# Optimization experiments

Hardware: AMD Instinct MI355X
Metric: run time of the kernel (lower is better)

## Reference

```python
import jax, jax.numpy as jnp
import numpy as np

B, C, H, W = 64, 256, 48, 48
NH = 8          # num_heads
DH = C // NH    # per-head dim = 32
DFF = 2 * C     # FFN hidden = 512 (hard-coded d_ffn=feature_dim*2)
M = 64          # base_class_num
EPS_NORM = 1e-5
EPS_LN = 1e-5


def setup_inputs() -> dict:
    key = jax.random.key(0)
    ks = jax.random.split(key, 12)
    s = 0.02
    return {
        "feature": jax.random.normal(ks[0], (B, C, H, W), jnp.float32),
        "base_class_weight": jax.random.normal(ks[1], (M, C), jnp.float32),
        # 1x1-conv projections (weight [out,in], bias [out])
        "wq": jax.random.normal(ks[2], (C, C), jnp.float32) * s,
        "bq": jnp.zeros((C,), jnp.float32),
        "wk": jax.random.normal(ks[3], (C, C), jnp.float32) * s,
        "bk": jnp.zeros((C,), jnp.float32),
        "wv": jax.random.normal(ks[4], (C, C), jnp.float32) * s,
        "bv": jnp.zeros((C,), jnp.float32),
        "wm": jax.random.normal(ks[5], (C, C), jnp.float32) * s,
        "bm": jnp.zeros((C,), jnp.float32),
        # FFN_MLP
        "w1": jax.random.normal(ks[6], (DFF, C), jnp.float32) * s,
        "b1": jnp.zeros((DFF,), jnp.float32),
        "w2": jax.random.normal(ks[7], (C, DFF), jnp.float32) * s,
        "b2": jnp.zeros((C,), jnp.float32),
        "gamma": jnp.ones((C,), jnp.float32),
        "beta": jnp.zeros((C,), jnp.float32),
    }


def reference(feature, base_class_weight, wq, bq, wk, bk, wv, bv, wm, bm,
              w1, b1, w2, b2, gamma, beta):
    b, c, h, w = feature.shape
    n = h * w
    feat_cn = feature.reshape(b, c, n)                 # [B,c,N]  (q input, channel-first)
    feat_nc = feat_cn.transpose(0, 2, 1)               # [B,N,c]  ('feature' var in torch)
    kv_cm = jnp.broadcast_to(base_class_weight.T[None], (b, c, M))  # [B,c,M]

    # 1x1-conv projections then split channels as [dim, heads] (dim outer, per torch view)
    qp = (jnp.einsum('oc,bcn->bon', wq, feat_cn) + bq[None, :, None]).reshape(b, DH, NH, n)
    kp = (jnp.einsum('oc,bcm->bom', wk, kv_cm) + bk[None, :, None]).reshape(b, DH, NH, M)
    vp = (jnp.einsum('oc,bcm->bom', wv, kv_cm) + bv[None, :, None]).reshape(b, DH, NH, M)

    scores = jnp.einsum('bdhn,bdhm->bhnm', qp, kp) / jnp.sqrt(jnp.float32(DH))
    prob = jax.nn.softmax(scores, axis=-1)             # [B,H,N,M]
    x = jnp.einsum('bhnm,bdhm->bdhn', prob, vp)        # [B,dim,H,N]
    merged = jnp.einsum('oc,bcn->bon', wm, x.reshape(b, c, n)) + bm[None, :, None]  # [B,c,N]

    # SFTA cosine re-weighting
    aligned = merged.transpose(0, 2, 1)                # [B,N,c]
    an = aligned / (jnp.linalg.norm(aligned, axis=-1, keepdims=True) + EPS_NORM)
    fn = feat_nc / (jnp.linalg.norm(feat_nc, axis=-1, keepdims=True) + EPS_NORM)
    cos = jnp.sum(an * fn, axis=-1)                    # [B,N]
    out = feat_nc * (cos + 1.0)[:, :, None]            # [B,N,c]

    # FFN_MLP (dropout = identity in eval) + residual + LayerNorm
    h1 = jax.nn.relu(jnp.einsum('bnc,fc->bnf', out, w1) + b1)
    src2 = jnp.einsum('bnf,cf->bnc', h1, w2) + b2
    src = out + src2
    mu = jnp.mean(src, axis=-1, keepdims=True)
    var = jnp.mean(jnp.square(src - mu), axis=-1, keepdims=True)
    src = (src - mu) / jnp.sqrt(var + EPS_LN) * gamma + beta

    return src.transpose(0, 2, 1).reshape(b, c, h, w)
```

## Files before the change

### kernel.cpp

```cpp
#include <hip/hip_runtime.h>

#define Bc   64
#define Cc   256
#define Nn   2304
#define DFFf 512
#define Mm   64
#define NTILE 64
#define NTB   36

typedef __bf16 bf16_t;
typedef __bf16 bf16x8 __attribute__((ext_vector_type(8)));
typedef __bf16 bf16x4 __attribute__((ext_vector_type(4)));
typedef float  f32x4  __attribute__((ext_vector_type(4)));
typedef float  f32x2  __attribute__((ext_vector_type(2)));

__device__ __forceinline__ bf16_t cvt(float f) { return (bf16_t)f; }

__device__ __forceinline__ f32x4 mfma16(bf16x8 a, bf16x8 b, f32x4 c) {
    return __builtin_amdgcn_mfma_f32_16x16x32_bf16(a, b, c, 0, 0, 0);
}

__global__ void kv_kernel(const float* __restrict__ wk, const float* __restrict__ bk,
                          const float* __restrict__ wv, const float* __restrict__ bv,
                          const float* __restrict__ bcw,
                          float* __restrict__ Kout, float* __restrict__ Vout) {
    int c = blockIdx.x;
    int m = threadIdx.x;
    const float* wkr = wk + c * Cc;
    const float* wvr = wv + c * Cc;
    const float* br  = bcw + m * Cc;
    float aK = 0.f, aV = 0.f;
    #pragma unroll 8
    for (int i = 0; i < Cc; ++i) {
        float bcv = br[i];
        aK = fmaf(wkr[i], bcv, aK);
        aV = fmaf(wvr[i], bcv, aV);
    }
    Kout[c * Mm + m] = aK + bk[c];
    Vout[c * Mm + m] = aV + bv[c];
}

__global__ void pack_kernel(const float* __restrict__ wq, const float* __restrict__ bq,
                            const float* __restrict__ wm, const float* __restrict__ w1,
                            const float* __restrict__ w2,
                            const float* __restrict__ Kf32, const float* __restrict__ Vf32,
                            bf16_t* __restrict__ wqf, bf16_t* __restrict__ wmf,
                            bf16_t* __restrict__ w1f, bf16_t* __restrict__ w2f,
                            bf16_t* __restrict__ Kf, bf16_t* __restrict__ Vf,
                            float* __restrict__ bqp) {
    int idx = blockIdx.x * 256 + threadIdx.x;
    if (idx < 65536) {
        int e = idx;
        int j = e & 7, lane = (e >> 3) & 63, rs = e >> 9;
        int ks = rs & 7, rt = rs >> 3;
        int rho = lane & 15;
        int h = rt >> 1, rtl = rt & 1;
        int d = 8 * (rho >> 2) + 4 * rtl + (rho & 3);
        int k  = ks * 32 + (lane >> 4) * 8 + j;
        int c  = d * 8 + h;
        wqf[e] = cvt(wq[c * 256 + k]);
    } else if (idx < 131072) {
        int e = idx - 65536;
        int j = e & 7, lane = (e >> 3) & 63, rs = e >> 9;
        int ks = rs & 7, rt = rs >> 3;
        int o = rt * 16 + (lane & 15);
        int k = ks * 32 + (lane >> 4) * 8 + j;
        int c = (k & 31) * 8 + (k >> 5);
        wmf[e] = cvt(wm[o * 256 + c]);
    } else if (idx < 262144) {
        int e = idx - 131072;
        int j = e & 7, lane = (e >> 3) & 63, rs = e >> 9;
        int ks = rs & 7, rt = rs >> 3;
        w1f[e] = cvt(w1[(rt * 16 + (lane & 15)) * 256 + ks * 32 + (lane >> 4) * 8 + j]);
    } else if (idx < 393216) {
        int e = idx - 262144;
        int j = e & 7, lane = (e >> 3) & 63, rs = e >> 9;
        int ks = rs & 15, rt = rs >> 4;
        w2f[e] = cvt(w2[(rt * 16 + (lane & 15)) * 512 + ks * 32 + (lane >> 4) * 8 + j]);
    } else if (idx < 409600) {
        int e = idx - 393216;
        int j = e & 7, lane = (e >> 3) & 63, hm = e >> 9;
        int mt = hm & 3, h = hm >> 2;
        int lid = lane & 15;
        int d = (lane >> 4) * 8 + j;
        int m = 32 * (mt >> 1) + 4 * (mt & 1) + 8 * (lid >> 2) + (lid & 3);
        Kf[e] = cvt(Kf32[(d * 8 + h) * 64 + m]);
    } else if (idx < 425984) {
        int e = idx - 409600;
        int j = e & 7, lane = (e >> 3) & 63, x = e >> 9;
        int ks = x & 1, rt = (x >> 1) & 1, h = x >> 2;
        int d = rt * 16 + (lane & 15), m = ks * 32 + (lane >> 4) * 8 + j;
        Vf[e] = cvt(Vf32[(d * 8 + h) * 64 + m]);
    } else if (idx < 426240) {
        int op = idx - 425984;
        int c = (op & 31) * 8 + (op >> 5);
        bqp[op] = bq[c];
    }
}

__global__ __launch_bounds__(1024, 8) void sfta_mfma(
    const float* __restrict__ feat,
    const bf16_t* __restrict__ wqf, const float* __restrict__ bqp,
    const bf16_t* __restrict__ wmf, const float* __restrict__ bm,
    const bf16_t* __restrict__ w1f, const float* __restrict__ b1,
    const bf16_t* __restrict__ w2f, const float* __restrict__ b2,
    const bf16_t* __restrict__ Kf,  const bf16_t* __restrict__ Vf,
    const float* __restrict__ gam,  const float* __restrict__ bet,
    float* __restrict__ out) {
    __shared__ __align__(16) bf16_t sFeat[64 * 264];
    __shared__ __align__(16) bf16_t sQX[64 * 264];
    __shared__ float sRed[3][64][18];

    const int t    = threadIdx.x;
    const int wid  = t >> 6;
    const int lane = t & 63;
    const int quad = lane >> 4;
    const int lid  = lane & 15;
    const int h    = wid >> 1;
    const int rtl  = wid & 1;
    const int b    = blockIdx.y;
    const int n0   = blockIdx.x * NTILE;
    const size_t baseF = (size_t)b * Cc * Nn + n0;

    {
        int cb = t >> 4;
        int nb = (t & 15) * 4;
        #pragma unroll
        for (int i = 0; i < 4; ++i) {
            int c = i * 64 + cb;
            const float4 f4 = *(const float4*)(feat + baseF + (size_t)c * Nn + nb);
            sFeat[(nb + 0) * 264 + c] = cvt(f4.x);
            sFeat[(nb + 1) * 264 + c] = cvt(f4.y);
            sFeat[(nb + 2) * 264 + c] = cvt(f4.z);
            sFeat[(nb + 3) * 264 + c] = cvt(f4.w);
        }
    }
    __syncthreads();

    {
        f32x4 qacc[4];
        #pragma unroll
        for (int nt = 0; nt < 4; ++nt) qacc[nt] = (f32x4){0.f, 0.f, 0.f, 0.f};
        #pragma unroll
        for (int ks = 0; ks < 8; ++ks) {
            bf16x8 a = *(const bf16x8*)(wqf + ((wid * 8 + ks) * 64 + lane) * 8);
            #pragma unroll
            for (int nt = 0; nt < 4; ++nt) {
                bf16x8 bfr = *(const bf16x8*)(sFeat + (nt * 16 + lid) * 264 + ks * 32 + quad * 8);
                qacc[nt] = mfma16(a, bfr, qacc[nt]);
            }
        }
        const float4 qb = *(const float4*)(bqp + h * 32 + quad * 8 + rtl * 4);
        #pragma unroll
        for (int nt = 0; nt < 4; ++nt) {
            bf16x4 o;
            o[0] = cvt(qacc[nt][0] + qb.x);
            o[1] = cvt(qacc[nt][1] + qb.y);
            o[2] = cvt(qacc[nt][2] + qb.z);
            o[3] = cvt(qacc[nt][3] + qb.w);
            *(bf16x4*)(sQX + (nt * 16 + lid) * 264 + h * 32 + quad * 8 + rtl * 4) = o;
        }
    }
    __syncthreads();

    {
        bf16x8 kb[4];
        #pragma unroll
        for (int mt = 0; mt < 4; ++mt)
            kb[mt] = *(const bf16x8*)(Kf + ((h * 4 + mt) * 64 + lane) * 8);
        const float scl2 = 0.17677669529663687f * 1.4426950408889634f;
        #pragma unroll 1
        for (int u = 0; u < 2; ++u) {
            int g = rtl * 2 + u;
            float p[16];
            {
                bf16x8 aq = *(const bf16x8*)(sQX + (g * 16 + lid) * 264 + h * 32 + quad * 8);
                #pragma unroll
                for (int mt = 0; mt < 4; ++mt) {
                    f32x4 z = {0.f, 0.f, 0.f, 0.f};
                    f32x4 sc = mfma16(kb[mt], aq, z);
                    #pragma unroll
                    for (int r = 0; r < 4; ++r) p[mt * 4 + r] = sc[r] * scl2;
                }
            }
            float mx = p[0];
            #pragma unroll
            for (int i = 1; i < 16; ++i) mx = fmaxf(mx, p[i]);
            mx = fmaxf(mx, __shfl_xor(mx, 16));
            mx = fmaxf(mx, __shfl_xor(mx, 32));
            float s = 0.f;
            #pragma unroll
            for (int i = 0; i < 16; ++i) { p[i] = exp2f(p[i] - mx); s += p[i]; }
            s += __shfl_xor(s, 16);
            s += __shfl_xor(s, 32);
            float inv = 1.f / s;
            bf16x8 bp[2];
            #pragma unroll
            for (int ks = 0; ks < 2; ++ks)
                #pragma unroll
                for (int jj = 0; jj < 8; ++jj)
                    bp[ks][jj] = cvt(p[(2 * ks + (jj >> 2)) * 4 + (jj & 3)] * inv);
            #pragma unroll
            for (int rv = 0; rv < 2; ++rv) {
                f32x4 x = {0.f, 0.f, 0.f, 0.f};
                bf16x8 va0 = *(const bf16x8*)(Vf + ((h * 4 + rv * 2 + 0) * 64 + lane) * 8);
                x = mfma16(va0, bp[0], x);
                bf16x8 va1 = *(const bf16x8*)(Vf + ((h * 4 + rv * 2 + 1) * 64 + lane) * 8);
                x = mfma16(va1, bp[1], x);
                bf16x4 o;
                #pragma unroll
                for (int r = 0; r < 4; ++r) o[r] = cvt(x[r]);
                *(bf16x4*)(sQX + (g * 16 + lid) * 264 + h * 32 + rv * 16 + quad * 4) = o;
            }
        }
    }
    __syncthreads();

    float pmf[4], pmm[4], pff[4];
    {
        f32x4 acc[4];
        #pragma unroll
        for (int nt = 0; nt < 4; ++nt) acc[nt] = (f32x4){0.f, 0.f, 0.f, 0.f};
        #pragma unroll
        for (int ks = 0; ks < 8; ++ks) {
            bf16x8 a = *(const bf16x8*)(wmf + ((wid * 8 + ks) * 64 + lane) * 8);
            #pragma unroll
            for (int nt = 0; nt < 4; ++nt) {
                bf16x8 bx = *(const bf16x8*)(sQX + (nt * 16 + lid) * 264 + ks * 32 + quad * 8);
                acc[nt] = mfma16(a, bx, acc[nt]);
            }
        }
        const float4 bmv = *(const float4*)(bm + wid * 16 + quad * 4);
        #pragma unroll
        for (int nt = 0; nt < 4; ++nt) { pmf[nt] = 0.f; pmm[nt] = 0.f; pff[nt] = 0.f; }
        #pragma unroll
        for (int nt = 0; nt < 4; ++nt) {
            bf16x4 f4 = *(const bf16x4*)(sFeat + (nt * 16 + lid) * 264 + wid * 16 + quad * 4);
            #pragma unroll
            for (int r = 0; r < 4; ++r) {
                float m = acc[nt][r] + ((const float*)&bmv)[r];
                float f = (float)f4[r];
                pmf[nt] = fmaf(m, f, pmf[nt]);
                pmm[nt] = fmaf(m, m, pmm[nt]);
                pff[nt] = fmaf(f, f, pff[nt]);
            }
        }
    }
    #pragma unroll
    for (int nt = 0; nt < 4; ++nt) {
        pmf[nt] += __shfl_xor(pmf[nt], 16); pmf[nt] += __shfl_xor(pmf[nt], 32);
        pmm[nt] += __shfl_xor(pmm[nt], 16); pmm[nt] += __shfl_xor(pmm[nt], 32);
        pff[nt] += __shfl_xor(pff[nt], 16); pff[nt] += __shfl_xor(pff[nt], 32);
    }
    if (lane < 16) {
        #pragma unroll
        for (int nt = 0; nt < 4; ++nt) {
            sRed[0][nt * 16 + lane][wid] = pmf[nt];
            sRed[1][nt * 16 + lane][wid] = pmm[nt];
            sRed[2][nt * 16 + lane][wid] = pff[nt];
        }
    }
    __syncthreads();

    {
        int row = wid * 4 + quad;
        float smf = 0.f, smm = 0.f, sff = 0.f;
        #pragma unroll
        for (int k2 = 0; k2 < 8; ++k2) {
            f32x2 a0 = *(const f32x2*)(&sRed[0][row][k2 * 2]);
            f32x2 a1 = *(const f32x2*)(&sRed[1][row][k2 * 2]);
            f32x2 a2 = *(const f32x2*)(&sRed[2][row][k2 * 2]);
            smf += a0[0] + a0[1];
            smm += a1[0] + a1[1];
            sff += a2[0] + a2[1];
        }
        float scale = smf / ((sqrtf(smm) + 1e-5f) * (sqrtf(sff) + 1e-5f)) + 1.f;
        bf16_t* frow = sFeat + row * 264 + lid * 16;
        #pragma unroll
        for (int i = 0; i < 2; ++i) {
            bf16x8* pp = (bf16x8*)(frow + i * 8);
            bf16x8 v = *pp;
            #pragma unroll
            for (int e = 0; e < 8; ++e) v[e] = cvt((float)v[e] * scale);
            *pp = v;
        }
    }
    __syncthreads();

    f32x4 acc2[4];
    #pragma unroll
    for (int nt = 0; nt < 4; ++nt) acc2[nt] = (f32x4){0.f, 0.f, 0.f, 0.f};
    #pragma unroll 1
    for (int c = 0; c < 2; ++c) {
        int rt1 = c * 16 + wid;
        {
            f32x4 a1[4];
            #pragma unroll
            for (int nt = 0; nt < 4; ++nt) a1[nt] = (f32x4){0.f, 0.f, 0.f, 0.f};
            #pragma unroll
            for (int ks = 0; ks < 8; ++ks) {
                bf16x8 a = *(const bf16x8*)(w1f + ((rt1 * 8 + ks) * 64 + lane) * 8);
                #pragma unroll
                for (int nt = 0; nt < 4; ++nt) {
                    bf16x8 bfr = *(const bf16x8*)(sFeat + (nt * 16 + lid) * 264 + ks * 32 + quad * 8);
                    a1[nt] = mfma16(a, bfr, a1[nt]);
                }
            }
            const float4 b1v = *(const float4*)(b1 + rt1 * 16 + quad * 4);
            #pragma unroll
            for (int nt = 0; nt < 4; ++nt) {
                bf16x4 o;
                o[0] = cvt(fmaxf(a1[nt][0] + b1v.x, 0.f));
                o[1] = cvt(fmaxf(a1[nt][1] + b1v.y, 0.f));
                o[2] = cvt(fmaxf(a1[nt][2] + b1v.z, 0.f));
                o[3] = cvt(fmaxf(a1[nt][3] + b1v.w, 0.f));
                *(bf16x4*)(sQX + (nt * 16 + lid) * 264 + wid * 16 + quad * 4) = o;
            }
        }
        __syncthreads();
        #pragma unroll
        for (int kk = 0; kk < 8; ++kk) {
            bf16x8 a = *(const bf16x8*)(w2f + ((wid * 16 + c * 8 + kk) * 64 + lane) * 8);
            #pragma unroll
            for (int nt = 0; nt < 4; ++nt) {
                bf16x8 bh = *(const bf16x8*)(sQX + (nt * 16 + lid) * 264 + kk * 32 + quad * 8);
                acc2[nt] = mfma16(a, bh, acc2[nt]);
            }
        }
        __syncthreads();
    }

    float ps[4] = {0.f, 0.f, 0.f, 0.f}, pq[4] = {0.f, 0.f, 0.f, 0.f};
    {
        const float4 b2v = *(const float4*)(b2 + wid * 16 + quad * 4);
        #pragma unroll
        for (int nt = 0; nt < 4; ++nt) {
            bf16x4 f4 = *(const bf16x4*)(sFeat + (nt * 16 + lid) * 264 + wid * 16 + quad * 4);
            #pragma unroll
            for (int r = 0; r < 4; ++r) {
                float v = acc2[nt][r] + ((const float*)&b2v)[r] + (float)f4[r];
                acc2[nt][r] = v;
                ps[nt] += v;
                pq[nt] = fmaf(v, v, pq[nt]);
            }
        }
    }
    #pragma unroll
    for (int nt = 0; nt < 4; ++nt) {
        ps[nt] += __shfl_xor(ps[nt], 16); ps[nt] += __shfl_xor(ps[nt], 32);
        pq[nt] += __shfl_xor(pq[nt], 16); pq[nt] += __shfl_xor(pq[nt], 32);
    }
    if (lane < 16) {
        #pragma unroll
        for (int nt = 0; nt < 4; ++nt) {
            sRed[0][nt * 16 + lane][wid] = ps[nt];
            sRed[1][nt * 16 + lane][wid] = pq[nt];
        }
    }
    __syncthreads();

    float* op = out + baseF;
    const float4 gv = *(const float4*)(gam + wid * 16 + quad * 4);
    const float4 bv = *(const float4*)(bet + wid * 16 + quad * 4);
    #pragma unroll
    for (int nt = 0; nt < 4; ++nt) {
        int row = nt * 16 + lid;
        float s = 0.f, q = 0.f;
        #pragma unroll
        for (int k2 = 0; k2 < 2; ++k2) {
            f32x2 a0 = *(const f32x2*)(&sRed[0][row][quad * 4 + k2 * 2]);
            f32x2 a1 = *(const f32x2*)(&sRed[1][row][quad * 4 + k2 * 2]);
            s += a0[0] + a0[1];
            q += a1[0] + a1[1];
        }
        s += __shfl_xor(s, 16); s += __shfl_xor(s, 32);
        q += __shfl_xor(q, 16); q += __shfl_xor(q, 32);
        float mu   = s * (1.f / 256.f);
        float rstd = rsqrtf(q * (1.f / 256.f) - mu * mu + 1e-5f);
        int ob = wid * 16 + quad * 4;
        #pragma unroll
        for (int r = 0; r < 4; ++r) {
            float y = (acc2[nt][r] - mu) * rstd * ((const float*)&gv)[r]
                      + ((const float*)&bv)[r];
            op[(size_t)(ob + r) * Nn + row] = y;
        }
    }
}

extern "C" void kernel_launch(void* const* d_in, const int* in_sizes, int n_in,
                              void* d_out, int out_size, void* d_ws, size_t ws_size,
                              hipStream_t stream) {
    const float* feature = (const float*)d_in[0];
    const float* bcw     = (const float*)d_in[1];
    const float* wq = (const float*)d_in[2];  const float* bq = (const float*)d_in[3];
    const float* wk = (const float*)d_in[4];  const float* bk = (const float*)d_in[5];
    const float* wv = (const float*)d_in[6];  const float* bv = (const float*)d_in[7];
    const float* wm = (const float*)d_in[8];  const float* bm = (const float*)d_in[9];
    const float* w1 = (const float*)d_in[10]; const float* b1 = (const float*)d_in[11];
    const float* w2 = (const float*)d_in[12]; const float* b2 = (const float*)d_in[13];
    const float* gm = (const float*)d_in[14]; const float* bt = (const float*)d_in[15];

    float*  Kf32 = (float*)d_ws;
    float*  Vf32 = Kf32 + 16384;
    bf16_t* wqf  = (bf16_t*)(Vf32 + 16384);
    bf16_t* wmf  = wqf + 65536;
    bf16_t* w1f  = wmf + 65536;
    bf16_t* w2f  = w1f + 131072;
    bf16_t* Kf   = w2f + 131072;
    bf16_t* Vf   = Kf + 16384;
    float*  bqp  = (float*)(Vf + 16384);

    float* op = (float*)d_out;

    hipLaunchKernelGGL(kv_kernel, dim3(Cc), dim3(Mm), 0, stream,
                       wk, bk, wv, bv, bcw, Kf32, Vf32);
    hipLaunchKernelGGL(pack_kernel, dim3((426240 + 255) / 256), dim3(256), 0, stream,
                       wq, bq, wm, w1, w2, Kf32, Vf32,
                       wqf, wmf, w1f, w2f, Kf, Vf, bqp);
    hipLaunchKernelGGL(sfta_mfma, dim3(NTB, Bc), dim3(1024), 0, stream,
                       feature, wqf, bqp, wmf, bm, w1f, b1, w2f, b2,
                       Kf, Vf, gm, bt, op);
}
```

Baseline: 464.4 us.

## Swizzle sFeat LDS layout and drop softmax max-subtraction with deferred normalization

```diff
diff --git a/kernel.cpp b/kernel.cpp
--- a/kernel.cpp
+++ b/kernel.cpp
@@ -18,6 +18,10 @@
 
 __device__ __forceinline__ f32x4 mfma16(bf16x8 a, bf16x8 b, f32x4 c) {
     return __builtin_amdgcn_mfma_f32_16x16x32_bf16(a, b, c, 0, 0, 0);
+}
+
+__device__ __forceinline__ int fsw(int row, int col) {
+    return row * 264 + (col ^ (((row >> 2) & 7) << 3));
 }
 
 __global__ void kv_kernel(const float* __restrict__ wk, const float* __restrict__ bk,
@@ -129,10 +133,10 @@
         for (int i = 0; i < 4; ++i) {
             int c = i * 64 + cb;
             const float4 f4 = *(const float4*)(feat + baseF + (size_t)c * Nn + nb);
-            sFeat[(nb + 0) * 264 + c] = cvt(f4.x);
-            sFeat[(nb + 1) * 264 + c] = cvt(f4.y);
-            sFeat[(nb + 2) * 264 + c] = cvt(f4.z);
-            sFeat[(nb + 3) * 264 + c] = cvt(f4.w);
+            sFeat[fsw(nb + 0, c)] = cvt(f4.x);
+            sFeat[fsw(nb + 1, c)] = cvt(f4.y);
+            sFeat[fsw(nb + 2, c)] = cvt(f4.z);
+            sFeat[fsw(nb + 3, c)] = cvt(f4.w);
         }
     }
     __syncthreads();
@@ -146,7 +150,7 @@
             bf16x8 a = *(const bf16x8*)(wqf + ((wid * 8 + ks) * 64 + lane) * 8);
             #pragma unroll
             for (int nt = 0; nt < 4; ++nt) {
-                bf16x8 bfr = *(const bf16x8*)(sFeat + (nt * 16 + lid) * 264 + ks * 32 + quad * 8);
+                bf16x8 bfr = *(const bf16x8*)(sFeat + fsw(nt * 16 + lid, ks * 32 + quad * 8));
                 qacc[nt] = mfma16(a, bfr, qacc[nt]);
             }
         }
@@ -172,34 +176,23 @@
         #pragma unroll 1
         for (int u = 0; u < 2; ++u) {
             int g = rtl * 2 + u;
-            float p[16];
-            {
-                bf16x8 aq = *(const bf16x8*)(sQX + (g * 16 + lid) * 264 + h * 32 + quad * 8);
+            bf16x8 aq = *(const bf16x8*)(sQX + (g * 16 + lid) * 264 + h * 32 + quad * 8);
+            float s = 0.f;
+            bf16x8 bp[2];
+            #pragma unroll
+            for (int mt = 0; mt < 4; ++mt) {
+                f32x4 z = {0.f, 0.f, 0.f, 0.f};
+                f32x4 sc = mfma16(kb[mt], aq, z);
                 #pragma unroll
-                for (int mt = 0; mt < 4; ++mt) {
-                    f32x4 z = {0.f, 0.f, 0.f, 0.f};
-                    f32x4 sc = mfma16(kb[mt], aq, z);
-                    #pragma unroll
-                    for (int r = 0; r < 4; ++r) p[mt * 4 + r] = sc[r] * scl2;
+                for (int r = 0; r < 4; ++r) {
+                    float e = exp2f(sc[r] * scl2);
+                    s += e;
+                    bp[mt >> 1][(mt & 1) * 4 + r] = cvt(e);
                 }
             }
-            float mx = p[0];
-            #pragma unroll
-            for (int i = 1; i < 16; ++i) mx = fmaxf(mx, p[i]);
-            mx = fmaxf(mx, __shfl_xor(mx, 16));
-            mx = fmaxf(mx, __shfl_xor(mx, 32));
-            float s = 0.f;
-            #pragma unroll
-            for (int i = 0; i < 16; ++i) { p[i] = exp2f(p[i] - mx); s += p[i]; }
             s += __shfl_xor(s, 16);
             s += __shfl_xor(s, 32);
             float inv = 1.f / s;
-            bf16x8 bp[2];
-            #pragma unroll
-            for (int ks = 0; ks < 2; ++ks)
-                #pragma unroll
-                for (int jj = 0; jj < 8; ++jj)
-                    bp[ks][jj] = cvt(p[(2 * ks + (jj >> 2)) * 4 + (jj & 3)] * inv);
             #pragma unroll
             for (int rv = 0; rv < 2; ++rv) {
                 f32x4 x = {0.f, 0.f, 0.f, 0.f};
@@ -209,7 +202,7 @@
                 x = mfma16(va1, bp[1], x);
                 bf16x4 o;
                 #pragma unroll
-                for (int r = 0; r < 4; ++r) o[r] = cvt(x[r]);
+                for (int r = 0; r < 4; ++r) o[r] = cvt(x[r] * inv);
                 *(bf16x4*)(sQX + (g * 16 + lid) * 264 + h * 32 + rv * 16 + quad * 4) = o;
             }
         }
@@ -235,7 +228,7 @@
         for (int nt = 0; nt < 4; ++nt) { pmf[nt] = 0.f; pmm[nt] = 0.f; pff[nt] = 0.f; }
         #pragma unroll
         for (int nt = 0; nt < 4; ++nt) {
-            bf16x4 f4 = *(const bf16x4*)(sFeat + (nt * 16 + lid) * 264 + wid * 16 + quad * 4);
+            bf16x4 f4 = *(const bf16x4*)(sFeat + fsw(nt * 16 + lid, wid * 16 + quad * 4));
             #pragma unroll
             for (int r = 0; r < 4; ++r) {
                 float m = acc[nt][r] + ((const float*)&bmv)[r];
@@ -275,10 +268,9 @@
             sff += a2[0] + a2[1];
         }
         float scale = smf / ((sqrtf(smm) + 1e-5f) * (sqrtf(sff) + 1e-5f)) + 1.f;
-        bf16_t* frow = sFeat + row * 264 + lid * 16;
         #pragma unroll
         for (int i = 0; i < 2; ++i) {
-            bf16x8* pp = (bf16x8*)(frow + i * 8);
+            bf16x8* pp = (bf16x8*)(sFeat + fsw(row, lid * 16 + i * 8));
             bf16x8 v = *pp;
             #pragma unroll
             for (int e = 0; e < 8; ++e) v[e] = cvt((float)v[e] * scale);
@@ -302,7 +294,7 @@
                 bf16x8 a = *(const bf16x8*)(w1f + ((rt1 * 8 + ks) * 64 + lane) * 8);
                 #pragma unroll
                 for (int nt = 0; nt < 4; ++nt) {
-                    bf16x8 bfr = *(const bf16x8*)(sFeat + (nt * 16 + lid) * 264 + ks * 32 + quad * 8);
+                    bf16x8 bfr = *(const bf16x8*)(sFeat + fsw(nt * 16 + lid, ks * 32 + quad * 8));
                     a1[nt] = mfma16(a, bfr, a1[nt]);
                 }
             }
@@ -335,7 +327,7 @@
         const float4 b2v = *(const float4*)(b2 + wid * 16 + quad * 4);
         #pragma unroll
         for (int nt = 0; nt < 4; ++nt) {
-            bf16x4 f4 = *(const bf16x4*)(sFeat + (nt * 16 + lid) * 264 + wid * 16 + quad * 4);
+            bf16x4 f4 = *(const bf16x4*)(sFeat + fsw(nt * 16 + lid, wid * 16 + quad * 4));
             #pragma unroll
             for (int r = 0; r < 4; ++r) {
                 float v = acc2[nt][r] + ((const float*)&b2v)[r] + (float)f4[r];
```

After: 534.0 us. 15.0% more time.
